# Kernel optimization log

Hardware: AMD Instinct MI355X
Metric: run time of the kernel (lower is better)

Reference implementation:

```python
import jax, jax.numpy as jnp
import numpy as np

D_TOK = 64
HID = 128


def _init_linear(key, fan_in, fan_out, bias_fill=None):
    kw, kb = jax.random.split(key)
    bound = 1.0 / np.sqrt(fan_in)
    W = jax.random.uniform(kw, (fan_in, fan_out), jnp.float32, -bound, bound)
    if bias_fill is None:
        b = jax.random.uniform(kb, (fan_out,), jnp.float32, -bound, bound)
    else:
        b = jnp.full((fan_out,), bias_fill, jnp.float32)
    return W, b


def setup_inputs() -> dict:
    key = jax.random.key(0)
    ks = jax.random.split(key, 7)
    N, E = 20000, 16
    tokens = jax.random.normal(ks[0], (N, E, D_TOK), jnp.float32)
    enc_W1, enc_b1 = _init_linear(ks[1], D_TOK, HID)
    enc_W2, enc_b2 = _init_linear(ks[2], HID, HID)
    spec_W1, spec_b1 = _init_linear(ks[3], 4 * HID, HID)
    spec_W2, spec_b2 = _init_linear(ks[4], HID, 1)
    def_W1, def_b1 = _init_linear(ks[5], 3 * HID, HID)
    def_W2, def_b2 = _init_linear(ks[6], HID, 1, bias_fill=-1.0)  # config.defer_bias
    return {
        "tokens": tokens,
        "enc_W1": enc_W1, "enc_b1": enc_b1, "enc_W2": enc_W2, "enc_b2": enc_b2,
        "spec_W1": spec_W1, "spec_b1": spec_b1, "spec_W2": spec_W2, "spec_b2": spec_b2,
        "def_W1": def_W1, "def_b1": def_b1, "def_W2": def_W2, "def_b2": def_b2,
        "full_index": 0,
        "top_k": 2,
    }


def _apply_top_k_mask(logits, full_index, top_k):
    # logits: [N, E]; mimic torch _apply_top_k_mask
    N, E = logits.shape
    if E <= 1:
        return logits
    neg = jnp.finfo(logits.dtype).min
    k = max(1, min(int(top_k), E - 1))
    masked = logits.at[:, full_index].set(neg)
    _, idx = jax.lax.top_k(masked, k)  # [N, k]
    rows = jnp.arange(N)[:, None]
    keep = jnp.zeros((N, E), bool).at[rows, idx].set(True)
    keep = keep.at[:, full_index].set(False)
    return jnp.where(keep, masked, neg)


def reference(tokens, enc_W1, enc_b1, enc_W2, enc_b2,
              spec_W1, spec_b1, spec_W2, spec_b2,
              def_W1, def_b1, def_W2, def_b2,
              full_index, top_k):
    neg = jnp.finfo(tokens.dtype).min
    # token encoder: two Linear+ReLU, applied per (row, expert)
    h = jax.nn.relu(tokens @ enc_W1 + enc_b1)
    encoded = jax.nn.relu(h @ enc_W2 + enc_b2)          # [N, E, H]
    full_token = encoded[:, full_index:full_index + 1]  # [N, 1, H]
    global_token = encoded.mean(axis=1, keepdims=True)  # [N, 1, H]
    token_delta = encoded - full_token
    global_delta = encoded - global_token
    pair = jnp.concatenate([encoded, token_delta, global_delta,
                            jnp.abs(token_delta)], axis=-1)  # [N, E, 4H]
    spec_h = jax.nn.relu(pair @ spec_W1 + spec_b1)
    specialist_logits = (spec_h @ spec_W2 + spec_b2)[..., 0]  # [N, E]
    specialist_logits = specialist_logits.at[:, full_index].set(neg)
    sparse_logits = _apply_top_k_mask(specialist_logits, full_index, top_k)
    w = jax.nn.softmax(sparse_logits, axis=1)
    w = w.at[:, full_index].set(0.0)
    mass = w.sum(axis=1, keepdims=True)
    w = jnp.where(mass > 0, w / jnp.maximum(mass, 1e-8), jnp.zeros_like(w))
    pooled = jnp.concatenate([full_token[:, 0], global_token[:, 0],
                              jnp.abs(token_delta).mean(axis=1)], axis=1)  # [N, 3H]
    def_h = jax.nn.relu(pooled @ def_W1 + def_b1)
    defer_prob = jax.nn.sigmoid(def_h @ def_W2 + def_b2)  # [N, 1]
    return w, defer_prob
```

## Files before the change

kernel.cpp:

```cpp
#include <hip/hip_runtime.h>
#include <math.h>

#define E 16
#define D 64
#define H 128
#define R 4
#define ROWS (R * E)
#define MW 16

__global__ void wabc_prep(const float* __restrict__ specW1, float* __restrict__ wabc) {
    int i = blockIdx.x * blockDim.x + threadIdx.x;
    if (i < H * H) {
        wabc[i] = specW1[i] + specW1[H * H + i] + specW1[2 * H * H + i];
    }
}

template <bool USE_WABC>
__global__ __launch_bounds__(256, 2)
void router_kernel(const float* __restrict__ tokens,
                   const float* __restrict__ encW1, const float* __restrict__ encB1,
                   const float* __restrict__ encW2, const float* __restrict__ encB2,
                   const float* __restrict__ specW1, const float* __restrict__ specB1,
                   const float* __restrict__ specW2,
                   const float* __restrict__ defW1, const float* __restrict__ defB1,
                   const float* __restrict__ defW2, const float* __restrict__ defB2,
                   const int* __restrict__ fiPtr, const int* __restrict__ tkPtr,
                   const float* __restrict__ wabc,
                   float* __restrict__ out, int N) {
    __shared__ float bufA[ROWS * H];
    __shared__ float bufB[ROWS * H];
    __shared__ float s_full[R * H];
    __shared__ float s_glob[R * H];
    __shared__ float s_mabs[R * H];
    __shared__ float s_bias[R * H];
    __shared__ float s_logits[ROWS];
    __shared__ float s_dred[R];

    const int tid   = threadIdx.x;
    const int n0    = blockIdx.x * R;
    const int fi    = fiPtr[0];
    const int lane  = tid & 63;
    const int wq    = tid >> 6;
    const int mbase = wq * MW;
    const int hw    = lane >> 5;
    const int jl    = lane & 31;
    const int jw0   = jl * 4;
    const int mb2   = mbase + hw * 8;

    {
        const size_t base  = (size_t)n0 * (E * D);
        const size_t total = (size_t)N * (E * D);
        float4* dst = (float4*)bufA;
#pragma unroll
        for (int it = 0; it < 4; it++) {
            int f = tid + it * 256;
            size_t off = base + (size_t)f * 4;
            float4 v = make_float4(0.f, 0.f, 0.f, 0.f);
            if (off + 3 < total) v = *(const float4*)(tokens + off);
            dst[f] = v;
        }
    }
    __syncthreads();

    {
        float acc[8][4];
#pragma unroll
        for (int m = 0; m < 8; m++)
#pragma unroll
            for (int j = 0; j < 4; j++) acc[m][j] = 0.f;
#pragma unroll 2
        for (int k = 0; k < D; k += 4) {
            float4 w0 = *(const float4*)(encW1 + (k + 0) * H + jw0);
            float4 w1 = *(const float4*)(encW1 + (k + 1) * H + jw0);
            float4 w2 = *(const float4*)(encW1 + (k + 2) * H + jw0);
            float4 w3 = *(const float4*)(encW1 + (k + 3) * H + jw0);
#pragma unroll
            for (int m = 0; m < 8; m++) {
                float4 t = *(const float4*)(bufA + (mb2 + m) * D + k);
                acc[m][0] = fmaf(t.w, w3.x, fmaf(t.z, w2.x, fmaf(t.y, w1.x, fmaf(t.x, w0.x, acc[m][0]))));
                acc[m][1] = fmaf(t.w, w3.y, fmaf(t.z, w2.y, fmaf(t.y, w1.y, fmaf(t.x, w0.y, acc[m][1]))));
                acc[m][2] = fmaf(t.w, w3.z, fmaf(t.z, w2.z, fmaf(t.y, w1.z, fmaf(t.x, w0.z, acc[m][2]))));
                acc[m][3] = fmaf(t.w, w3.w, fmaf(t.z, w2.w, fmaf(t.y, w1.w, fmaf(t.x, w0.w, acc[m][3]))));
            }
        }
        float4 b = *(const float4*)(encB1 + jw0);
#pragma unroll
        for (int m = 0; m < 8; m++) {
            float4 o;
            o.x = fmaxf(acc[m][0] + b.x, 0.f);
            o.y = fmaxf(acc[m][1] + b.y, 0.f);
            o.z = fmaxf(acc[m][2] + b.z, 0.f);
            o.w = fmaxf(acc[m][3] + b.w, 0.f);
            *(float4*)(bufB + (mb2 + m) * H + jw0) = o;
        }
    }
    __syncthreads();

    {
        float acc[8][4];
#pragma unroll
        for (int m = 0; m < 8; m++)
#pragma unroll
            for (int j = 0; j < 4; j++) acc[m][j] = 0.f;
#pragma unroll 2
        for (int k = 0; k < H; k += 4) {
            float4 w0 = *(const float4*)(encW2 + (k + 0) * H + jw0);
            float4 w1 = *(const float4*)(encW2 + (k + 1) * H + jw0);
            float4 w2 = *(const float4*)(encW2 + (k + 2) * H + jw0);
            float4 w3 = *(const float4*)(encW2 + (k + 3) * H + jw0);
#pragma unroll
            for (int m = 0; m < 8; m++) {
                float4 t = *(const float4*)(bufB + (mb2 + m) * H + k);
                acc[m][0] = fmaf(t.w, w3.x, fmaf(t.z, w2.x, fmaf(t.y, w1.x, fmaf(t.x, w0.x, acc[m][0]))));
                acc[m][1] = fmaf(t.w, w3.y, fmaf(t.z, w2.y, fmaf(t.y, w1.y, fmaf(t.x, w0.y, acc[m][1]))));
                acc[m][2] = fmaf(t.w, w3.z, fmaf(t.z, w2.z, fmaf(t.y, w1.z, fmaf(t.x, w0.z, acc[m][2]))));
                acc[m][3] = fmaf(t.w, w3.w, fmaf(t.z, w2.w, fmaf(t.y, w1.w, fmaf(t.x, w0.w, acc[m][3]))));
            }
        }
        float4 b = *(const float4*)(encB2 + jw0);
#pragma unroll
        for (int m = 0; m < 8; m++) {
            float4 o;
            o.x = fmaxf(acc[m][0] + b.x, 0.f);
            o.y = fmaxf(acc[m][1] + b.y, 0.f);
            o.z = fmaxf(acc[m][2] + b.z, 0.f);
            o.w = fmaxf(acc[m][3] + b.w, 0.f);
            *(float4*)(bufA + (mb2 + m) * H + jw0) = o;
        }
    }
    __syncthreads();

    {
        const int r4 = tid >> 6;
        const int cb = tid & 63;
#pragma unroll
        for (int half = 0; half < 2; half++) {
            const int c = cb + half * 64;
            const float* er = bufA + (r4 * E) * H + c;
            float v[E];
#pragma unroll
            for (int e = 0; e < E; e++) v[e] = er[e * H];
            float s = 0.f;
#pragma unroll
            for (int e = 0; e < E; e++) s += v[e];
            float fc = v[fi];
            float ma = 0.f;
#pragma unroll
            for (int e = 0; e < E; e++) ma += fabsf(v[e] - fc);
            s_full[r4 * H + c] = fc;
            s_glob[r4 * H + c] = s * (1.f / 16.f);
            s_mabs[r4 * H + c] = ma * (1.f / 16.f);
        }
    }
    __syncthreads();

    float* s_pB = bufB;
    float* s_pD = bufB + 2 * R * H;
    {
        const int jp = tid & 63;
        const int jj = jp * 2;
        const int kh = (tid >> 6) & 1;
        const int rg = tid >> 7;
        const int c0 = kh * 64;
        const float* __restrict__ Wb = specW1 + H * H;
        const float* __restrict__ Wc = specW1 + 2 * H * H;
        float accB[2][2] = {{0.f, 0.f}, {0.f, 0.f}};
        float accD[2][2] = {{0.f, 0.f}, {0.f, 0.f}};
        for (int cc = 0; cc < 64; cc++) {
            const int c = c0 + cc;
            float2 wb = *(const float2*)(Wb + c * H + jj);
            float2 wc = *(const float2*)(Wc + c * H + jj);
            float2 d0 = *(const float2*)(defW1 + c * H + jj);
            float2 d1 = *(const float2*)(defW1 + (H + c) * H + jj);
            float2 d2 = *(const float2*)(defW1 + (2 * H + c) * H + jj);
#pragma unroll
            for (int rl = 0; rl < 2; rl++) {
                const int r = rg * 2 + rl;
                float fv = s_full[r * H + c];
                float gv = s_glob[r * H + c];
                float mv = s_mabs[r * H + c];
                accB[rl][0] = fmaf(fv, wb.x, accB[rl][0]);
                accB[rl][1] = fmaf(fv, wb.y, accB[rl][1]);
                accB[rl][0] = fmaf(gv, wc.x, accB[rl][0]);
                accB[rl][1] = fmaf(gv, wc.y, accB[rl][1]);
                accD[rl][0] = fmaf(fv, d0.x, accD[rl][0]);
                accD[rl][1] = fmaf(fv, d0.y, accD[rl][1]);
                accD[rl][0] = fmaf(gv, d1.x, accD[rl][0]);
                accD[rl][1] = fmaf(gv, d1.y, accD[rl][1]);
                accD[rl][0] = fmaf(mv, d2.x, accD[rl][0]);
                accD[rl][1] = fmaf(mv, d2.y, accD[rl][1]);
            }
        }
#pragma unroll
        for (int rl = 0; rl < 2; rl++) {
            const int r = rg * 2 + rl;
            *(float2*)(s_pB + (kh * R + r) * H + jj) = make_float2(accB[rl][0], accB[rl][1]);
            *(float2*)(s_pD + (kh * R + r) * H + jj) = make_float2(accD[rl][0], accD[rl][1]);
        }
    }
    __syncthreads();

    {
        float dv = 0.f;
#pragma unroll
        for (int t = 0; t < 2; t++) {
            const int j = lane + t * 64;
            float pb = s_pB[wq * H + j] + s_pB[(R + wq) * H + j];
            s_bias[wq * H + j] = specB1[j] - pb;
            float pd = defB1[j] + s_pD[wq * H + j] + s_pD[(R + wq) * H + j];
            dv += fmaxf(pd, 0.f) * defW2[j];
        }
#pragma unroll
        for (int off = 32; off; off >>= 1) dv += __shfl_xor(dv, off, 64);
        if (lane == 0) s_dred[wq] = dv;
    }
    __syncthreads();

    {
        float acc[8][4];
#pragma unroll
        for (int m = 0; m < 8; m++)
#pragma unroll
            for (int j = 0; j < 4; j++) acc[m][j] = 0.f;
        const float* __restrict__ Wd = specW1 + 3 * H * H;
        for (int k = 0; k < H; k += 4) {
            float4 wa0, wa1, wa2, wa3;
            if (USE_WABC) {
                wa0 = *(const float4*)(wabc + (k + 0) * H + jw0);
                wa1 = *(const float4*)(wabc + (k + 1) * H + jw0);
                wa2 = *(const float4*)(wabc + (k + 2) * H + jw0);
                wa3 = *(const float4*)(wabc + (k + 3) * H + jw0);
            } else {
#pragma unroll
                for (int t = 0; t < 4; t++) {
                    const float* p = specW1 + (k + t) * H + jw0;
                    float4 x0 = *(const float4*)(p);
                    float4 x1 = *(const float4*)(p + H * H);
                    float4 x2 = *(const float4*)(p + 2 * H * H);
                    float4 s4 = make_float4(x0.x + x1.x + x2.x, x0.y + x1.y + x2.y,
                                            x0.z + x1.z + x2.z, x0.w + x1.w + x2.w);
                    if (t == 0) wa0 = s4; else if (t == 1) wa1 = s4;
                    else if (t == 2) wa2 = s4; else wa3 = s4;
                }
            }
            float4 wd0 = *(const float4*)(Wd + (k + 0) * H + jw0);
            float4 wd1 = *(const float4*)(Wd + (k + 1) * H + jw0);
            float4 wd2 = *(const float4*)(Wd + (k + 2) * H + jw0);
            float4 wd3 = *(const float4*)(Wd + (k + 3) * H + jw0);
            float4 f4 = *(const float4*)(s_full + wq * H + k);
#pragma unroll
            for (int m = 0; m < 8; m++) {
                float4 ev = *(const float4*)(bufA + (mb2 + m) * H + k);
                float ax = fabsf(ev.x - f4.x);
                float ay = fabsf(ev.y - f4.y);
                float az = fabsf(ev.z - f4.z);
                float aw = fabsf(ev.w - f4.w);
#pragma unroll
                for (int j = 0; j < 4; j++) {
                    const float* waj0 = &wa0.x, *waj1 = &wa1.x, *waj2 = &wa2.x, *waj3 = &wa3.x;
                    const float* wdj0 = &wd0.x, *wdj1 = &wd1.x, *wdj2 = &wd2.x, *wdj3 = &wd3.x;
                    float a = acc[m][j];
                    a = fmaf(ev.x, waj0[j], a);
                    a = fmaf(ev.y, waj1[j], a);
                    a = fmaf(ev.z, waj2[j], a);
                    a = fmaf(ev.w, waj3[j], a);
                    a = fmaf(ax, wdj0[j], a);
                    a = fmaf(ay, wdj1[j], a);
                    a = fmaf(az, wdj2[j], a);
                    a = fmaf(aw, wdj3[j], a);
                    acc[m][j] = a;
                }
            }
        }
        float4 bn = *(const float4*)(s_bias + wq * H + jw0);
        float4 w2 = *(const float4*)(specW2 + jw0);
#pragma unroll
        for (int m = 0; m < 8; m++) {
            float p = 0.f;
            p += fmaxf(acc[m][0] + bn.x, 0.f) * w2.x;
            p += fmaxf(acc[m][1] + bn.y, 0.f) * w2.y;
            p += fmaxf(acc[m][2] + bn.z, 0.f) * w2.z;
            p += fmaxf(acc[m][3] + bn.w, 0.f) * w2.w;
#pragma unroll
            for (int off = 1; off < 32; off <<= 1) p += __shfl_xor(p, off, 64);
            if (jl == 0) s_logits[mb2 + m] = p;
        }
    }
    __syncthreads();

    if (tid < R && (n0 + tid) < N) {
        const int r = tid;
        const int n = n0 + r;
        float s = s_dred[r] + defB2[0];
        out[(size_t)N * E + n] = 1.f / (1.f + expf(-s));
        int k = tkPtr[0];
        if (k < 1) k = 1;
        if (k > E - 1) k = E - 1;
        unsigned chosen = 0u;
        for (int kk = 0; kk < k; kk++) {
            float bv = -INFINITY;
            int bi = 0;
            for (int e = 0; e < E; e++) {
                if (e == fi || ((chosen >> e) & 1u)) continue;
                float v = s_logits[r * E + e];
                if (v > bv) { bv = v; bi = e; }
            }
            chosen |= (1u << bi);
        }
        float mx = -INFINITY;
        for (int e = 0; e < E; e++)
            if ((chosen >> e) & 1u) { float v = s_logits[r * E + e]; if (v > mx) mx = v; }
        float ssum = 0.f;
        for (int e = 0; e < E; e++)
            if ((chosen >> e) & 1u) ssum += expf(s_logits[r * E + e] - mx);
        float inv = 1.f / ssum;
        for (int e = 0; e < E; e++) {
            float wv = 0.f;
            if ((chosen >> e) & 1u) wv = expf(s_logits[r * E + e] - mx) * inv;
            out[(size_t)n * E + e] = wv;
        }
    }
}

extern "C" void kernel_launch(void* const* d_in, const int* in_sizes, int n_in,
                              void* d_out, int out_size, void* d_ws, size_t ws_size,
                              hipStream_t stream) {
    (void)n_in; (void)out_size;
    const float* tokens = (const float*)d_in[0];
    const float* encW1  = (const float*)d_in[1];
    const float* encB1  = (const float*)d_in[2];
    const float* encW2  = (const float*)d_in[3];
    const float* encB2  = (const float*)d_in[4];
    const float* specW1 = (const float*)d_in[5];
    const float* specB1 = (const float*)d_in[6];
    const float* specW2 = (const float*)d_in[7];
    const float* defW1  = (const float*)d_in[9];
    const float* defB1  = (const float*)d_in[10];
    const float* defW2  = (const float*)d_in[11];
    const float* defB2  = (const float*)d_in[12];
    const int*   fiPtr  = (const int*)d_in[13];
    const int*   tkPtr  = (const int*)d_in[14];
    float* out = (float*)d_out;

    const int N = in_sizes[0] / (E * D);
    const int grid = (N + R - 1) / R;
    const bool useWs = (d_ws != nullptr) && (ws_size >= (size_t)(H * H * sizeof(float)));

    if (useWs) {
        wabc_prep<<<(H * H + 255) / 256, 256, 0, stream>>>(specW1, (float*)d_ws);
        router_kernel<true><<<grid, 256, 0, stream>>>(
            tokens, encW1, encB1, encW2, encB2, specW1, specB1, specW2,
            defW1, defB1, defW2, defB2, fiPtr, tkPtr, (const float*)d_ws, out, N);
    } else {
        router_kernel<false><<<grid, 256, 0, stream>>>(
            tokens, encW1, encB1, encW2, encB2, specW1, specB1, specW2,
            defW1, defB1, defW2, defB2, fiPtr, tkPtr, nullptr, out, N);
    }
}
```

Baseline: 747.9 us.

## Make each wave own one row, replacing block barriers with wave barriers

Restructures the router kernel so each 64-lane wave processes one token row end to end in its own shared-memory slice. This replaces every __syncthreads with wave-level barriers and reuses a single buffer in place instead of double buffering. The pooled/bias/defer stage now reduces via cross-half shuffles in registers, and launch bounds rise to 4 blocks per CU. The aim is to cut block-wide synchronisation and LDS footprint to raise occupancy. In exchange, the in-place buffer reuse depends on wave barriers and register pressure under the tighter launch bound.

```diff
diff --git a/kernel.cpp b/kernel.cpp
--- a/kernel.cpp
+++ b/kernel.cpp
@@ -5,8 +5,6 @@
 #define D 64
 #define H 128
 #define R 4
-#define ROWS (R * E)
-#define MW 16
 
 __global__ void wabc_prep(const float* __restrict__ specW1, float* __restrict__ wabc) {
     int i = blockIdx.x * blockDim.x + threadIdx.x;
@@ -16,7 +14,7 @@
 }
 
 template <bool USE_WABC>
-__global__ __launch_bounds__(256, 2)
+__global__ __launch_bounds__(256, 4)
 void router_kernel(const float* __restrict__ tokens,
                    const float* __restrict__ encW1, const float* __restrict__ encB1,
                    const float* __restrict__ encW2, const float* __restrict__ encB2,
@@ -27,40 +25,30 @@
                    const int* __restrict__ fiPtr, const int* __restrict__ tkPtr,
                    const float* __restrict__ wabc,
                    float* __restrict__ out, int N) {
-    __shared__ float bufA[ROWS * H];
-    __shared__ float bufB[ROWS * H];
+    __shared__ float buf[R * E * H];
     __shared__ float s_full[R * H];
     __shared__ float s_glob[R * H];
     __shared__ float s_mabs[R * H];
-    __shared__ float s_bias[R * H];
-    __shared__ float s_logits[ROWS];
-    __shared__ float s_dred[R];
-
-    const int tid   = threadIdx.x;
-    const int n0    = blockIdx.x * R;
-    const int fi    = fiPtr[0];
-    const int lane  = tid & 63;
-    const int wq    = tid >> 6;
-    const int mbase = wq * MW;
-    const int hw    = lane >> 5;
-    const int jl    = lane & 31;
-    const int jw0   = jl * 4;
-    const int mb2   = mbase + hw * 8;
-
-    {
-        const size_t base  = (size_t)n0 * (E * D);
-        const size_t total = (size_t)N * (E * D);
-        float4* dst = (float4*)bufA;
-#pragma unroll
-        for (int it = 0; it < 4; it++) {
-            int f = tid + it * 256;
-            size_t off = base + (size_t)f * 4;
-            float4 v = make_float4(0.f, 0.f, 0.f, 0.f);
-            if (off + 3 < total) v = *(const float4*)(tokens + off);
-            dst[f] = v;
-        }
-    }
-    __syncthreads();
+
+    const int tid  = threadIdx.x;
+    const int lane = tid & 63;
+    const int wq   = tid >> 6;
+    const int n    = blockIdx.x * R + wq;
+    if (n >= N) return;
+
+    const int fi  = fiPtr[0];
+    const int hw  = lane >> 5;
+    const int jl  = lane & 31;
+    const int jw0 = jl * 4;
+    float* __restrict__ wbuf = buf + wq * (E * H);
+
+    {
+        const float4* __restrict__ src = (const float4*)(tokens + (size_t)n * (E * D));
+        float4* dst = (float4*)wbuf;
+#pragma unroll
+        for (int it = 0; it < 4; it++) dst[lane + it * 64] = src[lane + it * 64];
+    }
+    __builtin_amdgcn_wave_barrier();
 
     {
         float acc[8][4];
@@ -76,7 +64,7 @@
             float4 w3 = *(const float4*)(encW1 + (k + 3) * H + jw0);
 #pragma unroll
             for (int m = 0; m < 8; m++) {
-                float4 t = *(const float4*)(bufA + (mb2 + m) * D + k);
+                float4 t = *(const float4*)(wbuf + (hw * 8 + m) * D + k);
                 acc[m][0] = fmaf(t.w, w3.x, fmaf(t.z, w2.x, fmaf(t.y, w1.x, fmaf(t.x, w0.x, acc[m][0]))));
                 acc[m][1] = fmaf(t.w, w3.y, fmaf(t.z, w2.y, fmaf(t.y, w1.y, fmaf(t.x, w0.y, acc[m][1]))));
                 acc[m][2] = fmaf(t.w, w3.z, fmaf(t.z, w2.z, fmaf(t.y, w1.z, fmaf(t.x, w0.z, acc[m][2]))));
@@ -84,6 +72,7 @@
             }
         }
         float4 b = *(const float4*)(encB1 + jw0);
+        __builtin_amdgcn_wave_barrier();
 #pragma unroll
         for (int m = 0; m < 8; m++) {
             float4 o;
@@ -91,10 +80,10 @@
             o.y = fmaxf(acc[m][1] + b.y, 0.f);
             o.z = fmaxf(acc[m][2] + b.z, 0.f);
             o.w = fmaxf(acc[m][3] + b.w, 0.f);
-            *(float4*)(bufB + (mb2 + m) * H + jw0) = o;
-        }
-    }
-    __syncthreads();
+            *(float4*)(wbuf + (hw * 8 + m) * H + jw0) = o;
+        }
+    }
+    __builtin_amdgcn_wave_barrier();
 
     {
         float acc[8][4];
@@ -110,7 +99,7 @@
             float4 w3 = *(const float4*)(encW2 + (k + 3) * H + jw0);
 #pragma unroll
             for (int m = 0; m < 8; m++) {
-                float4 t = *(const float4*)(bufB + (mb2 + m) * H + k);
+                float4 t = *(const float4*)(wbuf + (hw * 8 + m) * H + k);
                 acc[m][0] = fmaf(t.w, w3.x, fmaf(t.z, w2.x, fmaf(t.y, w1.x, fmaf(t.x, w0.x, acc[m][0]))));
                 acc[m][1] = fmaf(t.w, w3.y, fmaf(t.z, w2.y, fmaf(t.y, w1.y, fmaf(t.x, w0.y, acc[m][1]))));
                 acc[m][2] = fmaf(t.w, w3.z, fmaf(t.z, w2.z, fmaf(t.y, w1.z, fmaf(t.x, w0.z, acc[m][2]))));
@@ -118,6 +107,7 @@
             }
         }
         float4 b = *(const float4*)(encB2 + jw0);
+        __builtin_amdgcn_wave_barrier();
 #pragma unroll
         for (int m = 0; m < 8; m++) {
             float4 o;
@@ -125,96 +115,74 @@
             o.y = fmaxf(acc[m][1] + b.y, 0.f);
             o.z = fmaxf(acc[m][2] + b.z, 0.f);
             o.w = fmaxf(acc[m][3] + b.w, 0.f);
-            *(float4*)(bufA + (mb2 + m) * H + jw0) = o;
-        }
-    }
-    __syncthreads();
-
-    {
-        const int r4 = tid >> 6;
-        const int cb = tid & 63;
-#pragma unroll
-        for (int half = 0; half < 2; half++) {
-            const int c = cb + half * 64;
-            const float* er = bufA + (r4 * E) * H + c;
-            float v[E];
-#pragma unroll
-            for (int e = 0; e < E; e++) v[e] = er[e * H];
-            float s = 0.f;
-#pragma unroll
-            for (int e = 0; e < E; e++) s += v[e];
-            float fc = v[fi];
-            float ma = 0.f;
-#pragma unroll
-            for (int e = 0; e < E; e++) ma += fabsf(v[e] - fc);
-            s_full[r4 * H + c] = fc;
-            s_glob[r4 * H + c] = s * (1.f / 16.f);
-            s_mabs[r4 * H + c] = ma * (1.f / 16.f);
-        }
-    }
-    __syncthreads();
-
-    float* s_pB = bufB;
-    float* s_pD = bufB + 2 * R * H;
-    {
-        const int jp = tid & 63;
-        const int jj = jp * 2;
-        const int kh = (tid >> 6) & 1;
-        const int rg = tid >> 7;
-        const int c0 = kh * 64;
+            *(float4*)(wbuf + (hw * 8 + m) * H + jw0) = o;
+        }
+    }
+    __builtin_amdgcn_wave_barrier();
+
+    {
+        const int c2 = lane * 2;
+        float2 fc = *(const float2*)(wbuf + fi * H + c2);
+        float sx = 0.f, sy = 0.f, mx = 0.f, my = 0.f;
+#pragma unroll
+        for (int e = 0; e < E; e++) {
+            float2 v = *(const float2*)(wbuf + e * H + c2);
+            sx += v.x; sy += v.y;
+            mx += fabsf(v.x - fc.x); my += fabsf(v.y - fc.y);
+        }
+        *(float2*)(s_full + wq * H + c2) = fc;
+        *(float2*)(s_glob + wq * H + c2) = make_float2(sx * 0.0625f, sy * 0.0625f);
+        *(float2*)(s_mabs + wq * H + c2) = make_float2(mx * 0.0625f, my * 0.0625f);
+    }
+    __builtin_amdgcn_wave_barrier();
+
+    float4 biasr;
+    {
         const float* __restrict__ Wb = specW1 + H * H;
         const float* __restrict__ Wc = specW1 + 2 * H * H;
-        float accB[2][2] = {{0.f, 0.f}, {0.f, 0.f}};
-        float accD[2][2] = {{0.f, 0.f}, {0.f, 0.f}};
+        const int c0 = hw * 64;
+        float accB[4] = {0.f, 0.f, 0.f, 0.f};
+        float accD[4] = {0.f, 0.f, 0.f, 0.f};
+#pragma unroll 2
         for (int cc = 0; cc < 64; cc++) {
             const int c = c0 + cc;
-            float2 wb = *(const float2*)(Wb + c * H + jj);
-            float2 wc = *(const float2*)(Wc + c * H + jj);
-            float2 d0 = *(const float2*)(defW1 + c * H + jj);
-            float2 d1 = *(const float2*)(defW1 + (H + c) * H + jj);
-            float2 d2 = *(const float2*)(defW1 + (2 * H + c) * H + jj);
-#pragma unroll
-            for (int rl = 0; rl < 2; rl++) {
-                const int r = rg * 2 + rl;
-                float fv = s_full[r * H + c];
-                float gv = s_glob[r * H + c];
-                float mv = s_mabs[r * H + c];
-                accB[rl][0] = fmaf(fv, wb.x, accB[rl][0]);
-                accB[rl][1] = fmaf(fv, wb.y, accB[rl][1]);
-                accB[rl][0] = fmaf(gv, wc.x, accB[rl][0]);
-                accB[rl][1] = fmaf(gv, wc.y, accB[rl][1]);
-                accD[rl][0] = fmaf(fv, d0.x, accD[rl][0]);
-                accD[rl][1] = fmaf(fv, d0.y, accD[rl][1]);
-                accD[rl][0] = fmaf(gv, d1.x, accD[rl][0]);
-                accD[rl][1] = fmaf(gv, d1.y, accD[rl][1]);
-                accD[rl][0] = fmaf(mv, d2.x, accD[rl][0]);
-                accD[rl][1] = fmaf(mv, d2.y, accD[rl][1]);
-            }
-        }
-#pragma unroll
-        for (int rl = 0; rl < 2; rl++) {
-            const int r = rg * 2 + rl;
-            *(float2*)(s_pB + (kh * R + r) * H + jj) = make_float2(accB[rl][0], accB[rl][1]);
-            *(float2*)(s_pD + (kh * R + r) * H + jj) = make_float2(accD[rl][0], accD[rl][1]);
-        }
-    }
-    __syncthreads();
-
-    {
-        float dv = 0.f;
-#pragma unroll
-        for (int t = 0; t < 2; t++) {
-            const int j = lane + t * 64;
-            float pb = s_pB[wq * H + j] + s_pB[(R + wq) * H + j];
-            s_bias[wq * H + j] = specB1[j] - pb;
-            float pd = defB1[j] + s_pD[wq * H + j] + s_pD[(R + wq) * H + j];
-            dv += fmaxf(pd, 0.f) * defW2[j];
-        }
-#pragma unroll
-        for (int off = 32; off; off >>= 1) dv += __shfl_xor(dv, off, 64);
-        if (lane == 0) s_dred[wq] = dv;
-    }
-    __syncthreads();
+            float4 wb = *(const float4*)(Wb + c * H + jw0);
+            float4 wc = *(const float4*)(Wc + c * H + jw0);
+            float4 d0 = *(const float4*)(defW1 + c * H + jw0);
+            float4 d1 = *(const float4*)(defW1 + (H + c) * H + jw0);
+            float4 d2 = *(const float4*)(defW1 + (2 * H + c) * H + jw0);
+            float fv = s_full[wq * H + c];
+            float gv = s_glob[wq * H + c];
+            float mv = s_mabs[wq * H + c];
+            accB[0] = fmaf(gv, wc.x, fmaf(fv, wb.x, accB[0]));
+            accB[1] = fmaf(gv, wc.y, fmaf(fv, wb.y, accB[1]));
+            accB[2] = fmaf(gv, wc.z, fmaf(fv, wb.z, accB[2]));
+            accB[3] = fmaf(gv, wc.w, fmaf(fv, wb.w, accB[3]));
+            accD[0] = fmaf(mv, d2.x, fmaf(gv, d1.x, fmaf(fv, d0.x, accD[0])));
+            accD[1] = fmaf(mv, d2.y, fmaf(gv, d1.y, fmaf(fv, d0.y, accD[1])));
+            accD[2] = fmaf(mv, d2.z, fmaf(gv, d1.z, fmaf(fv, d0.z, accD[2])));
+            accD[3] = fmaf(mv, d2.w, fmaf(gv, d1.w, fmaf(fv, d0.w, accD[3])));
+        }
+#pragma unroll
+        for (int t = 0; t < 4; t++) {
+            accB[t] += __shfl_xor(accB[t], 32, 64);
+            accD[t] += __shfl_xor(accD[t], 32, 64);
+        }
+        float4 sb = *(const float4*)(specB1 + jw0);
+        biasr = make_float4(sb.x - accB[0], sb.y - accB[1], sb.z - accB[2], sb.w - accB[3]);
+        float4 db = *(const float4*)(defB1 + jw0);
+        float4 dw = *(const float4*)(defW2 + jw0);
+        float dv = fmaxf(db.x + accD[0], 0.f) * dw.x
+                 + fmaxf(db.y + accD[1], 0.f) * dw.y
+                 + fmaxf(db.z + accD[2], 0.f) * dw.z
+                 + fmaxf(db.w + accD[3], 0.f) * dw.w;
+#pragma unroll
+        for (int off = 1; off < 32; off <<= 1) dv += __shfl_xor(dv, off, 64);
+        if (lane == 0) {
+            float s = dv + defB2[0];
+            out[(size_t)N * E + n] = 1.f / (1.f + expf(-s));
+        }
+    }
 
     {
         float acc[8][4];
@@ -250,7 +218,7 @@
             float4 f4 = *(const float4*)(s_full + wq * H + k);
 #pragma unroll
             for (int m = 0; m < 8; m++) {
-                float4 ev = *(const float4*)(bufA + (mb2 + m) * H + k);
+                float4 ev = *(const float4*)(wbuf + (hw * 8 + m) * H + k);
                 float ax = fabsf(ev.x - f4.x);
                 float ay = fabsf(ev.y - f4.y);
                 float az = fabsf(ev.z - f4.z);
@@ -272,27 +240,23 @@
                 }
             }
         }
-        float4 bn = *(const float4*)(s_bias + wq * H + jw0);
         float4 w2 = *(const float4*)(specW2 + jw0);
+        __builtin_amdgcn_wave_barrier();
 #pragma unroll
         for (int m = 0; m < 8; m++) {
             float p = 0.f;
-            p += fmaxf(acc[m][0] + bn.x, 0.f) * w2.x;
-            p += fmaxf(acc[m][1] + bn.y, 0.f) * w2.y;
-            p += fmaxf(acc[m][2] + bn.z, 0.f) * w2.z;
-            p += fmaxf(acc[m][3] + bn.w, 0.f) * w2.w;
+            p += fmaxf(acc[m][0] + biasr.x, 0.f) * w2.x;
+            p += fmaxf(acc[m][1] + biasr.y, 0.f) * w2.y;
+            p += fmaxf(acc[m][2] + biasr.z, 0.f) * w2.z;
+            p += fmaxf(acc[m][3] + biasr.w, 0.f) * w2.w;
 #pragma unroll
             for (int off = 1; off < 32; off <<= 1) p += __shfl_xor(p, off, 64);
-            if (jl == 0) s_logits[mb2 + m] = p;
-        }
-    }
-    __syncthreads();
-
-    if (tid < R && (n0 + tid) < N) {
-        const int r = tid;
-        const int n = n0 + r;
-        float s = s_dred[r] + defB2[0];
-        out[(size_t)N * E + n] = 1.f / (1.f + expf(-s));
+            if (jl == 0) wbuf[hw * 8 + m] = p;
+        }
+    }
+    __builtin_amdgcn_wave_barrier();
+
+    if (lane == 0) {
         int k = tkPtr[0];
         if (k < 1) k = 1;
         if (k > E - 1) k = E - 1;
@@ -302,21 +266,21 @@
             int bi = 0;
             for (int e = 0; e < E; e++) {
                 if (e == fi || ((chosen >> e) & 1u)) continue;
-                float v = s_logits[r * E + e];
+                float v = wbuf[e];
                 if (v > bv) { bv = v; bi = e; }
             }
             chosen |= (1u << bi);
         }
         float mx = -INFINITY;
         for (int e = 0; e < E; e++)
-            if ((chosen >> e) & 1u) { float v = s_logits[r * E + e]; if (v > mx) mx = v; }
+            if ((chosen >> e) & 1u) { float v = wbuf[e]; if (v > mx) mx = v; }
         float ssum = 0.f;
         for (int e = 0; e < E; e++)
-            if ((chosen >> e) & 1u) ssum += expf(s_logits[r * E + e] - mx);
+            if ((chosen >> e) & 1u) ssum += expf(wbuf[e] - mx);
         float inv = 1.f / ssum;
         for (int e = 0; e < E; e++) {
             float wv = 0.f;
-            if ((chosen >> e) & 1u) wv = expf(s_logits[r * E + e] - mx) * inv;
+            if ((chosen >> e) & 1u) wv = expf(wbuf[e] - mx) * inv;
             out[(size_t)n * E + e] = wv;
         }
     }
```

Result: faster. 724.1 us (-3.2%).
